# Kernel optimization log

Measured on AMD Instinct MI355X. Metric: run time of the kernel, lower is better.

The kernel has to match this reference:

```python
import jax, jax.numpy as jnp
import numpy as np

E = 16   # n_experts
K = 4    # top_k
NEG = jnp.float32(-1e20)


def _swiglu(x, w1, w2, w3):
    # bias-free SwiGLU expert: (swish(x@w1) * (x@w2)) @ w3
    a = x @ w1
    return (a * jax.nn.sigmoid(a) * (x @ w2)) @ w3


def setup_inputs() -> dict:
    key = jax.random.key(0)
    ks = jax.random.split(key, 9)
    B, S, D, H = 32, 512, 512, 1365  # H = D*2*4//3
    s = 0.02  # weight init scale to keep activations sane
    return {
        "x": jax.random.normal(ks[0], (B, S, D), jnp.float32),
        "gate_w": jax.random.normal(ks[1], (D, E), jnp.float32) * s,
        "routing_bias": jnp.zeros((E,), jnp.float32),
        "w1": jax.random.normal(ks[2], (E, D, H), jnp.float32) * s,
        "w2": jax.random.normal(ks[3], (E, D, H), jnp.float32) * s,
        "w3": jax.random.normal(ks[4], (E, H, D), jnp.float32) * s,
        "sw1": jax.random.normal(ks[5], (D, H), jnp.float32) * s,
        "sw2": jax.random.normal(ks[6], (D, H), jnp.float32) * s,
        "sw3": jax.random.normal(ks[7], (H, D), jnp.float32) * s,
    }


def reference(x, gate_w, routing_bias, w1, w2, w3, sw1, sw2, sw3):
    # gate logits + aux-free load-balancing bias  [B,S,E]
    gate_out = x @ gate_w + routing_bias
    top_v, top_i = jax.lax.top_k(gate_out, K)
    # chosen[b,s,e] = 1 if expert e is in the top-k for token (b,s)
    chosen = jax.nn.one_hot(top_i, E, dtype=x.dtype).sum(axis=-2)
    # scatter top-k values onto a -1e20 background, then softmax over experts
    masked = jnp.where(chosen > 0, gate_out, NEG)
    probs = jax.nn.softmax(masked, axis=-1)
    weights = probs * chosen  # zero outside the chosen set (matches torch mask)
    # shared expert runs on all tokens
    out = _swiglu(x, sw1, sw2, sw3)
    # per-expert SwiGLU, weighted-combined (loop over fixed small E)
    for e in range(E):
        out = out + _swiglu(x, w1[e], w2[e], w3[e]) * weights[..., e:e + 1]
    return out
```

## Files before the change

### kernel.cpp

```cpp
#include <hip/hip_runtime.h>

#define NT    16384
#define DDIM  512
#define HDIM  1365
#define HPAD  1408
#define NEXP  16
#define BK    64
#define BM    128
#define MAXTILES 656
#define MAXSLOTS 83968

typedef unsigned short u16;
typedef unsigned int   u32;
typedef __attribute__((ext_vector_type(8))) __bf16 bf16x8;
typedef __attribute__((ext_vector_type(4))) float  f32x4;
typedef __attribute__((address_space(3))) void lds_void;
typedef __attribute__((address_space(1))) void glb_void;

__device__ __forceinline__ u16 f2bf(float f) {
  union { float f; u32 u; } v; v.f = f;
  u32 u = v.u;
  u += 0x7fffu + ((u >> 16) & 1u);
  return (u16)(u >> 16);
}

__device__ __forceinline__ float bf2f(u16 b) {
  union { u32 u; float f; } v; v.u = ((u32)b) << 16;
  return v.f;
}

__device__ __forceinline__ f32x4 mfma16(bf16x8 a, bf16x8 b, f32x4 c) {
  return __builtin_amdgcn_mfma_f32_16x16x32_bf16(a, b, c, 0, 0, 0);
}

__device__ __forceinline__ void gload16(const u16* g, u16* l) {
  __builtin_amdgcn_global_load_lds((const glb_void*)g, (lds_void*)l, 16, 0, 0);
}

__device__ __forceinline__ bf16x8 lds_frag(const u16* base, int row, int e0) {
  int b = ((row << 7) + (e0 << 1)) ^ ((row & 7) << 4);
  return *(const bf16x8*)((const char*)base + b);
}

__device__ __forceinline__ int swz_n(int bid, int n) {
  int q = n >> 3, r = n & 7;
  int xcd = bid & 7, j = bid >> 3;
  return (xcd < r ? xcd * (q + 1) : r * (q + 1) + (xcd - r) * q) + j;
}

__global__ void convert_x_kernel(const float* __restrict__ in, u16* __restrict__ out, int n8) {
  int i = blockIdx.x * 256 + threadIdx.x;
  if (i >= n8) return;
  float4 a = ((const float4*)in)[2 * i];
  float4 b = ((const float4*)in)[2 * i + 1];
  u16 r[8] = {f2bf(a.x), f2bf(a.y), f2bf(a.z), f2bf(a.w),
              f2bf(b.x), f2bf(b.y), f2bf(b.z), f2bf(b.w)};
  ((uint4*)out)[i] = *(const uint4*)r;
}

__global__ void transpose12_kernel(const float* __restrict__ in, u16* __restrict__ out) {
  __shared__ float tile[32][65];
  int e = blockIdx.z;
  int h0 = blockIdx.x * 32, d0 = blockIdx.y * 64;
  int tx = threadIdx.x, ty = threadIdx.y;
  int h = h0 + tx;
#pragma unroll
  for (int r = 0; r < 8; ++r) {
    int d = d0 + ty + r * 8;
    float v = (h < HDIM) ? in[((size_t)e * DDIM + d) * HDIM + h] : 0.f;
    tile[tx][ty + r * 8] = v;
  }
  __syncthreads();
#pragma unroll
  for (int r = 0; r < 4; ++r) {
    int hh = h0 + ty + r * 8;
    u32 lo = f2bf(tile[ty + r * 8][2 * tx]);
    u32 hi = f2bf(tile[ty + r * 8][2 * tx + 1]);
    ((u32*)&out[((size_t)e * HPAD + hh) * DDIM + d0])[tx] = lo | (hi << 16);
  }
}

__global__ void transpose3_kernel(const float* __restrict__ in, u16* __restrict__ out) {
  __shared__ float tile[32][65];
  int e = blockIdx.z;
  int h0 = blockIdx.x * 64, d0 = blockIdx.y * 32;
  int tx = threadIdx.x, ty = threadIdx.y;
  int d = d0 + tx;
#pragma unroll
  for (int r = 0; r < 8; ++r) {
    int h = h0 + ty + r * 8;
    float v = (h < HDIM) ? in[((size_t)e * HDIM + h) * DDIM + d] : 0.f;
    tile[tx][ty + r * 8] = v;
  }
  __syncthreads();
#pragma unroll
  for (int r = 0; r < 4; ++r) {
    int dd = d0 + ty + r * 8;
    u32 lo = f2bf(tile[ty + r * 8][2 * tx]);
    u32 hi = f2bf(tile[ty + r * 8][2 * tx + 1]);
    ((u32*)&out[((size_t)e * DDIM + dd) * HPAD + h0])[tx] = lo | (hi << 16);
  }
}

__global__ __launch_bounds__(512) void routing_kernel(
    const float* __restrict__ x, const float* __restrict__ gw,
    const float* __restrict__ rbias,
    int* __restrict__ top_e, float* __restrict__ top_w) {
  __shared__ float gwT[NEXP * DDIM];
  int tid = threadIdx.x;
  for (int i = tid; i < NEXP * DDIM; i += 512) {
    int d = i >> 4, e = i & 15;
    gwT[e * DDIM + d] = gw[i];
  }
  __syncthreads();
  int w = tid >> 6, lane = tid & 63;
  int t = blockIdx.x * 8 + w;
  const float* xr = x + (size_t)t * DDIM;
  float xv[8];
#pragma unroll
  for (int k = 0; k < 8; ++k) xv[k] = xr[lane + (k << 6)];
  float acc[NEXP];
#pragma unroll
  for (int e = 0; e < NEXP; ++e) {
    const float* ge = gwT + e * DDIM + lane;
    float s = 0.f;
#pragma unroll
    for (int k = 0; k < 8; ++k) s += xv[k] * ge[k << 6];
#pragma unroll
    for (int off = 32; off; off >>= 1) s += __shfl_xor(s, off);
    acc[e] = s + rbias[e];
  }
  if (lane == 0) {
    int sel[4]; float sv[4];
    unsigned used = 0;
#pragma unroll
    for (int i = 0; i < 4; ++i) {
      float best = -1e30f; int bi = 0;
#pragma unroll
      for (int e = 0; e < NEXP; ++e) {
        bool ok = !((used >> e) & 1u) && acc[e] > best;
        best = ok ? acc[e] : best;
        bi   = ok ? e : bi;
      }
      used |= 1u << bi; sel[i] = bi; sv[i] = best;
    }
    float m = sv[0];
    float ex[4]; float s = 0.f;
#pragma unroll
    for (int i = 0; i < 4; ++i) { ex[i] = __expf(sv[i] - m); s += ex[i]; }
    float inv = 1.f / s;
#pragma unroll
    for (int i = 0; i < 4; ++i) {
      top_e[t * 4 + i] = sel[i];
      top_w[t * 4 + i] = ex[i] * inv;
    }
  }
}

__global__ __launch_bounds__(1024) void rank_kernel(const int* __restrict__ top_e,
                                                    int* __restrict__ counts,
                                                    int* __restrict__ top_pos) {
  __shared__ int hist[NEXP], base[NEXP];
  int tid = threadIdx.x;
  int t = blockIdx.x * 1024 + tid;
  if (tid < NEXP) hist[tid] = 0;
  __syncthreads();
  int e4[4], r4[4];
#pragma unroll
  for (int i = 0; i < 4; ++i) {
    e4[i] = top_e[t * 4 + i];
    r4[i] = atomicAdd(&hist[e4[i]], 1);
  }
  __syncthreads();
  if (tid < NEXP) base[tid] = atomicAdd(&counts[tid], hist[tid]);
  __syncthreads();
#pragma unroll
  for (int i = 0; i < 4; ++i) top_pos[t * 4 + i] = base[e4[i]] + r4[i];
}

__global__ void finalize_kernel(const int* __restrict__ counts, int* __restrict__ slot_off,
                                int* __restrict__ ntiles, int2* __restrict__ desc) {
  if (threadIdx.x != 0) return;
  int off = 0, td = 0;
  for (int e = 0; e < 17; ++e) {
    int c = (e == 16) ? NT : counts[e];
    slot_off[e] = off;
    int nt = (c + BM - 1) / BM;
    for (int i = 0; i < nt; ++i) { desc[td] = make_int2(e, off + i * BM); ++td; }
    off += nt * BM;
  }
  slot_off[17] = off;
  *ntiles = td;
}

__global__ void scatter_kernel(const int* __restrict__ top_e, const float* __restrict__ top_w,
                               const int* __restrict__ top_pos, const int* __restrict__ slot_off,
                               int* __restrict__ tok_pad, float* __restrict__ w_pad,
                               int* __restrict__ pos_list) {
  int t = blockIdx.x * 256 + threadIdx.x;
  if (t >= NT) return;
#pragma unroll
  for (int i = 0; i < 4; ++i) {
    int e = top_e[t * 4 + i];
    int slot = slot_off[e] + top_pos[t * 4 + i];
    tok_pad[slot] = t;
    w_pad[slot] = top_w[t * 4 + i];
    pos_list[t * 4 + i] = slot;
  }
  int sh = slot_off[16] + t;
  tok_pad[sh] = t;
  w_pad[sh] = 1.f;
}

__global__ __launch_bounds__(256, 3) void gemm1_kernel(
    const u16* __restrict__ x_bf, const u16* __restrict__ w1t, const u16* __restrict__ w2t,
    const u16* __restrict__ sw1t, const u16* __restrict__ sw2t,
    const int* __restrict__ ntiles, const int2* __restrict__ desc,
    const int* __restrict__ tok_pad, u16* __restrict__ h, int lo, int ntc) {
  int ti = (lo >> 7) + swz_n(blockIdx.x, ntc);
  if (ti >= *ntiles) return;
  int2 de = desc[ti];
  int e = de.x, m0 = de.y;
  int n0 = blockIdx.y * 64;
  const u16* W1 = (e == 16) ? sw1t : (w1t + (size_t)e * HPAD * DDIM);
  const u16* W2 = (e == 16) ? sw2t : (w2t + (size_t)e * HPAD * DDIM);

  __shared__ u16 smem[16384];
  u16* xs = smem;
  u16* bs = smem + 8192;

  int tid = threadIdx.x, w = tid >> 6, lane = tid & 63;
  int wm = w >> 1, wn = w & 1, lr = lane & 15, lk = lane >> 4;

  const u16* ags[4]; const u16* bgs[4];
  int ce = (((lane & 7) ^ ((lane >> 3) & 7)) << 3);
#pragma unroll
  for (int p = 0; p < 4; ++p) {
    int r = w * 32 + p * 8 + (lane >> 3);
    ags[p] = x_bf + (size_t)tok_pad[m0 + r] * DDIM + ce;
    int grp = (w * 32 + p * 8) >> 4;
    const u16* Wsrc = (grp & 1) ? W2 : W1;
    int hrow = n0 + ((grp >> 1) << 4) + (r & 15);
    bgs[p] = Wsrc + (size_t)hrow * DDIM + ce;
  }

  f32x4 acc[4][4] = {};

  for (int ks = 0; ks < DDIM / BK; ++ks) {
    int k0 = ks * BK;
#pragma unroll
    for (int p = 0; p < 4; ++p) {
      gload16(ags[p] + k0, xs + ((w * 32 + p * 8) << 6));
      gload16(bgs[p] + k0, bs + ((w * 32 + p * 8) << 6));
    }
    __syncthreads();
#pragma unroll
    for (int kf = 0; kf < 2; ++kf) {
      int e0 = kf * 32 + lk * 8;
      bf16x8 bfr[4];
#pragma unroll
      for (int nf = 0; nf < 4; ++nf)
        bfr[nf] = lds_frag(bs, wn * 64 + nf * 16 + lr, e0);
#pragma unroll
      for (int mf = 0; mf < 4; ++mf) {
        bf16x8 a = lds_frag(xs, wm * 64 + mf * 16 + lr, e0);
#pragma unroll
        for (int nf = 0; nf < 4; ++nf)
          acc[mf][nf] = mfma16(a, bfr[nf], acc[mf][nf]);
      }
    }
    __syncthreads();
  }

  u16* hs = smem;
#pragma unroll
  for (int mf = 0; mf < 4; ++mf)
#pragma unroll
    for (int nf = 0; nf < 4; nf += 2)
#pragma unroll
      for (int j = 0; j < 4; ++j) {
        float g = acc[mf][nf][j], u = acc[mf][nf + 1][j];
        float hv = g * u / (1.f + __expf(-g));
        int row = wm * 64 + mf * 16 + lk * 4 + j;
        int col = wn * 32 + (nf >> 1) * 16 + lr;
        hs[(row << 6) + col] = f2bf(hv);
      }
  __syncthreads();
#pragma unroll
  for (int i = 0; i < 4; ++i) {
    int idx = (i * 256 + tid) * 8;
    int row = idx >> 6, col = idx & 63;
    *(uint4*)&h[(size_t)(m0 - lo + row) * HPAD + n0 + col] = *(uint4*)&hs[idx];
  }
}

template <bool YMODE>
__global__ __launch_bounds__(256, 3) void gemm2_kernel(
    const u16* __restrict__ h, const u16* __restrict__ w3t, const u16* __restrict__ sw3t,
    const int* __restrict__ ntiles, const int2* __restrict__ desc,
    const int* __restrict__ tok_pad, const float* __restrict__ w_pad,
    u16* __restrict__ y, float* __restrict__ out, int lo, int ntc) {
  int ti = (lo >> 7) + swz_n(blockIdx.x, ntc);
  if (ti >= *ntiles) return;
  int2 de = desc[ti];
  int e = de.x, m0 = de.y;
  int n0 = blockIdx.y * 128;
  const u16* W3 = (e == 16) ? sw3t : (w3t + (size_t)e * DDIM * HPAD);

  __shared__ u16 smem[16384];
  __shared__ float swl[BM];
  u16* hs = smem;
  u16* ws3 = smem + 8192;

  int tid = threadIdx.x, w = tid >> 6, lane = tid & 63;
  int wm = w >> 1, wn = w & 1, lr = lane & 15, lk = lane >> 4;

  if (tid < BM) swl[tid] = w_pad[m0 + tid];

  const u16* ags[4]; const u16* bgs[4];
  int ce = (((lane & 7) ^ ((lane >> 3) & 7)) << 3);
#pragma unroll
  for (int p = 0; p < 4; ++p) {
    int r = w * 32 + p * 8 + (lane >> 3);
    ags[p] = h + (size_t)(m0 - lo + r) * HPAD + ce;
    bgs[p] = W3 + (size_t)(n0 + r) * HPAD + ce;
  }

  f32x4 acc[4][4] = {};

  for (int ks = 0; ks < HPAD / BK; ++ks) {
    int k0 = ks * BK;
#pragma unroll
    for (int p = 0; p < 4; ++p) {
      gload16(ags[p] + k0, hs + ((w * 32 + p * 8) << 6));
      gload16(bgs[p] + k0, ws3 + ((w * 32 + p * 8) << 6));
    }
    __syncthreads();
#pragma unroll
    for (int kf = 0; kf < 2; ++kf) {
      int e0 = kf * 32 + lk * 8;
      bf16x8 bfr[4];
#pragma unroll
      for (int nf = 0; nf < 4; ++nf)
        bfr[nf] = lds_frag(ws3, wn * 64 + nf * 16 + lr, e0);
#pragma unroll
      for (int mf = 0; mf < 4; ++mf) {
        bf16x8 a = lds_frag(hs, wm * 64 + mf * 16 + lr, e0);
#pragma unroll
        for (int nf = 0; nf < 4; ++nf)
          acc[mf][nf] = mfma16(a, bfr[nf], acc[mf][nf]);
      }
    }
    __syncthreads();
  }

  if constexpr (YMODE) {
    u16* ys = smem;
#pragma unroll
    for (int mf = 0; mf < 4; ++mf)
#pragma unroll
      for (int j = 0; j < 4; ++j) {
        int row = wm * 64 + mf * 16 + lk * 4 + j;
        float wv = swl[row];
#pragma unroll
        for (int nf = 0; nf < 4; ++nf)
          ys[(row << 7) + wn * 64 + nf * 16 + lr] = f2bf(acc[mf][nf][j] * wv);
      }
    __syncthreads();
#pragma unroll
    for (int i = 0; i < 8; ++i) {
      int idx = (i * 256 + tid) * 8;
      int row = idx >> 7, col = idx & 127;
      *(uint4*)&y[(size_t)(m0 + row) * DDIM + n0 + col] = *(uint4*)&ys[idx];
    }
  } else {
#pragma unroll
    for (int mf = 0; mf < 4; ++mf)
#pragma unroll
      for (int j = 0; j < 4; ++j) {
        int row = wm * 64 + mf * 16 + lk * 4 + j;
        float wv = swl[row];
        float* orow = out + (size_t)tok_pad[m0 + row] * DDIM + n0;
#pragma unroll
        for (int nf = 0; nf < 4; ++nf)
          atomicAdd(&orow[wn * 64 + nf * 16 + lr], acc[mf][nf][j] * wv);
      }
  }
}

__global__ void reduce_kernel(const u16* __restrict__ y, const int* __restrict__ pos_list,
                              const int* __restrict__ slot_off, float* __restrict__ out) {
  int t = blockIdx.x;
  int c = threadIdx.x;
  int4 pl = ((const int4*)pos_list)[t];
  int sh = slot_off[16] + t;
  ushort4 a = ((const ushort4*)(y + (size_t)sh * DDIM))[c];
  ushort4 b = ((const ushort4*)(y + (size_t)pl.x * DDIM))[c];
  ushort4 d = ((const ushort4*)(y + (size_t)pl.y * DDIM))[c];
  ushort4 e = ((const ushort4*)(y + (size_t)pl.z * DDIM))[c];
  ushort4 f = ((const ushort4*)(y + (size_t)pl.w * DDIM))[c];
  float4 s;
  s.x = bf2f(a.x) + bf2f(b.x) + bf2f(d.x) + bf2f(e.x) + bf2f(f.x);
  s.y = bf2f(a.y) + bf2f(b.y) + bf2f(d.y) + bf2f(e.y) + bf2f(f.y);
  s.z = bf2f(a.z) + bf2f(b.z) + bf2f(d.z) + bf2f(e.z) + bf2f(f.z);
  s.w = bf2f(a.w) + bf2f(b.w) + bf2f(d.w) + bf2f(e.w) + bf2f(f.w);
  ((float4*)(out + (size_t)t * DDIM))[c] = s;
}

extern "C" void kernel_launch(void* const* d_in, const int* in_sizes, int n_in,
                              void* d_out, int out_size, void* d_ws, size_t ws_size,
                              hipStream_t stream) {
  const float* x      = (const float*)d_in[0];
  const float* gate_w = (const float*)d_in[1];
  const float* rbias  = (const float*)d_in[2];
  const float* w1     = (const float*)d_in[3];
  const float* w2     = (const float*)d_in[4];
  const float* w3     = (const float*)d_in[5];
  const float* sw1    = (const float*)d_in[6];
  const float* sw2    = (const float*)d_in[7];
  const float* sw3    = (const float*)d_in[8];
  float* out = (float*)d_out;

  char* ws = (char*)d_ws;
  size_t off = 0;
  auto alloc = [&](size_t bytes) -> char* {
    char* p = ws + off;
    off += (bytes + 255) & ~(size_t)255;
    return p;
  };
  u16* x_bf  = (u16*)alloc((size_t)NT * DDIM * 2);
  u16* w1t   = (u16*)alloc((size_t)NEXP * HPAD * DDIM * 2);
  u16* w2t   = (u16*)alloc((size_t)NEXP * HPAD * DDIM * 2);
  u16* w3t   = (u16*)alloc((size_t)NEXP * DDIM * HPAD * 2);
  u16* sw1t  = (u16*)alloc((size_t)HPAD * DDIM * 2);
  u16* sw2t  = (u16*)alloc((size_t)HPAD * DDIM * 2);
  u16* sw3t  = (u16*)alloc((size_t)DDIM * HPAD * 2);
  int*   counts   = (int*)alloc(64 * 4);
  int*   top_e    = (int*)alloc((size_t)NT * 4 * 4);
  float* top_w    = (float*)alloc((size_t)NT * 4 * 4);
  int*   top_pos  = (int*)alloc((size_t)NT * 4 * 4);
  int*   slot_off = (int*)alloc(32 * 4);
  int*   ntiles   = (int*)alloc(256);
  int2*  desc     = (int2*)alloc((size_t)MAXTILES * 8);
  int*   tok_pad  = (int*)alloc((size_t)MAXSLOTS * 4);
  float* w_pad    = (float*)alloc((size_t)MAXSLOTS * 4);
  int*   pos_list = (int*)alloc((size_t)NT * 4 * 4);
  size_t y_off = off;
  u16* y = (u16*)alloc((size_t)MAXSLOTS * DDIM * 2);
  size_t h_off_y = off;
  (void)in_sizes; (void)n_in; (void)ws_size;

  const size_t per_row = (size_t)HPAD * 2;
  bool ymode;
  size_t h_off, rows_avail;
  size_t avail_y = (ws_size > h_off_y) ? (ws_size - h_off_y) : 0;
  if (avail_y / per_row >= 10496) {
    ymode = true; h_off = h_off_y; rows_avail = avail_y / per_row;
  } else {
    ymode = false; h_off = y_off;
    size_t avail_a = (ws_size > y_off) ? (ws_size - y_off) : 0;
    rows_avail = avail_a / per_row;
  }
  int CS;
  if (rows_avail >= (size_t)MAXSLOTS) CS = MAXSLOTS;
  else {
    CS = (int)((rows_avail / 2048) * 2048);
    if (CS < 2048) CS = (int)((rows_avail / BM) * BM);
    if (CS < BM) CS = BM;
  }
  int NCH = (MAXSLOTS + CS - 1) / CS;
  u16* h = (u16*)(ws + h_off);

  hipMemsetAsync(counts, 0, 64 * 4, stream);
  hipMemsetAsync(tok_pad, 0, (size_t)MAXSLOTS * 4, stream);
  hipMemsetAsync(w_pad, 0, (size_t)MAXSLOTS * 4, stream);
  if (!ymode) hipMemsetAsync(out, 0, (size_t)out_size * 4, stream);

  int n8 = NT * DDIM / 8;
  convert_x_kernel<<<n8 / 256, 256, 0, stream>>>(x, x_bf, n8);

  dim3 tb(32, 8);
  transpose12_kernel<<<dim3(HPAD / 32, DDIM / 64, NEXP), tb, 0, stream>>>(w1, w1t);
  transpose12_kernel<<<dim3(HPAD / 32, DDIM / 64, NEXP), tb, 0, stream>>>(w2, w2t);
  transpose12_kernel<<<dim3(HPAD / 32, DDIM / 64, 1),    tb, 0, stream>>>(sw1, sw1t);
  transpose12_kernel<<<dim3(HPAD / 32, DDIM / 64, 1),    tb, 0, stream>>>(sw2, sw2t);
  transpose3_kernel<<<dim3(HPAD / 64, DDIM / 32, NEXP),  tb, 0, stream>>>(w3, w3t);
  transpose3_kernel<<<dim3(HPAD / 64, DDIM / 32, 1),     tb, 0, stream>>>(sw3, sw3t);

  routing_kernel<<<NT / 8, 512, 0, stream>>>(x, gate_w, rbias, top_e, top_w);
  rank_kernel<<<NT / 1024, 1024, 0, stream>>>(top_e, counts, top_pos);
  finalize_kernel<<<1, 64, 0, stream>>>(counts, slot_off, ntiles, desc);
  scatter_kernel<<<NT / 256, 256, 0, stream>>>(top_e, top_w, top_pos, slot_off,
                                               tok_pad, w_pad, pos_list);

  for (int c = 0; c < NCH; ++c) {
    int lo = c * CS;
    int ntc = (MAXSLOTS - lo < CS ? MAXSLOTS - lo : CS) >> 7;
    gemm1_kernel<<<dim3(ntc, HPAD / 64), 256, 0, stream>>>(
        x_bf, w1t, w2t, sw1t, sw2t, ntiles, desc, tok_pad, h, lo, ntc);
    if (ymode)
      gemm2_kernel<true><<<dim3(ntc, DDIM / 128), 256, 0, stream>>>(
          h, w3t, sw3t, ntiles, desc, tok_pad, w_pad, y, out, lo, ntc);
    else
      gemm2_kernel<false><<<dim3(ntc, DDIM / 128), 256, 0, stream>>>(
          h, w3t, sw3t, ntiles, desc, tok_pad, w_pad, y, out, lo, ntc);
  }
  if (ymode) reduce_kernel<<<NT, 128, 0, stream>>>(y, pos_list, slot_off, out);
}
```

Before: 642.4 us.

## Fuse x conversion into routing, merge transpose launches, linearize GEMM grids, swizzle epilogue LDS

Folds the fp32-to-bf16 conversion of x into the routing kernel, which now reads x with vectorized loads and uses a permuted gate-weight layout in LDS. The six weight-transpose launches become two, each selecting its source tensor by blockIdx.z. The GEMM grids are flattened to 1D, and the XCD swizzle now covers every (token tile, column block) pair so neighbouring tiles sharing weights land on the same XCD. The epilogue LDS staging gets an XOR swizzle to cut bank conflicts. Together these aim to reduce launch count, global memory passes and L2 misses, at the cost of slightly more index arithmetic.

Result: faster. 615.0 us (-4.3%).

```diff
diff --git a/kernel.cpp b/kernel.cpp
--- a/kernel.cpp
+++ b/kernel.cpp
@@ -48,26 +48,24 @@
   return (xcd < r ? xcd * (q + 1) : r * (q + 1) + (xcd - r) * q) + j;
 }
 
-__global__ void convert_x_kernel(const float* __restrict__ in, u16* __restrict__ out, int n8) {
-  int i = blockIdx.x * 256 + threadIdx.x;
-  if (i >= n8) return;
-  float4 a = ((const float4*)in)[2 * i];
-  float4 b = ((const float4*)in)[2 * i + 1];
-  u16 r[8] = {f2bf(a.x), f2bf(a.y), f2bf(a.z), f2bf(a.w),
-              f2bf(b.x), f2bf(b.y), f2bf(b.z), f2bf(b.w)};
-  ((uint4*)out)[i] = *(const uint4*)r;
-}
-
-__global__ void transpose12_kernel(const float* __restrict__ in, u16* __restrict__ out) {
+__global__ void transpose12_kernel(const float* __restrict__ w1, const float* __restrict__ w2,
+                                   const float* __restrict__ sw1, const float* __restrict__ sw2,
+                                   u16* __restrict__ w1t, u16* __restrict__ w2t,
+                                   u16* __restrict__ sw1t, u16* __restrict__ sw2t) {
   __shared__ float tile[32][65];
-  int e = blockIdx.z;
+  int z = blockIdx.z;
+  const float* in; u16* out;
+  if (z < 16)      { in = w1 + (size_t)z * DDIM * HDIM;        out = w1t + (size_t)z * HPAD * DDIM; }
+  else if (z < 32) { in = w2 + (size_t)(z - 16) * DDIM * HDIM; out = w2t + (size_t)(z - 16) * HPAD * DDIM; }
+  else if (z == 32){ in = sw1; out = sw1t; }
+  else             { in = sw2; out = sw2t; }
   int h0 = blockIdx.x * 32, d0 = blockIdx.y * 64;
   int tx = threadIdx.x, ty = threadIdx.y;
   int h = h0 + tx;
 #pragma unroll
   for (int r = 0; r < 8; ++r) {
     int d = d0 + ty + r * 8;
-    float v = (h < HDIM) ? in[((size_t)e * DDIM + d) * HDIM + h] : 0.f;
+    float v = (h < HDIM) ? in[(size_t)d * HDIM + h] : 0.f;
     tile[tx][ty + r * 8] = v;
   }
   __syncthreads();
@@ -76,20 +74,23 @@
     int hh = h0 + ty + r * 8;
     u32 lo = f2bf(tile[ty + r * 8][2 * tx]);
     u32 hi = f2bf(tile[ty + r * 8][2 * tx + 1]);
-    ((u32*)&out[((size_t)e * HPAD + hh) * DDIM + d0])[tx] = lo | (hi << 16);
-  }
-}
-
-__global__ void transpose3_kernel(const float* __restrict__ in, u16* __restrict__ out) {
+    ((u32*)&out[(size_t)hh * DDIM + d0])[tx] = lo | (hi << 16);
+  }
+}
+
+__global__ void transpose3_kernel(const float* __restrict__ w3, const float* __restrict__ sw3,
+                                  u16* __restrict__ w3t, u16* __restrict__ sw3t) {
   __shared__ float tile[32][65];
-  int e = blockIdx.z;
+  int z = blockIdx.z;
+  const float* in = (z < 16) ? (w3 + (size_t)z * HDIM * DDIM) : sw3;
+  u16* out = (z < 16) ? (w3t + (size_t)z * DDIM * HPAD) : sw3t;
   int h0 = blockIdx.x * 64, d0 = blockIdx.y * 32;
   int tx = threadIdx.x, ty = threadIdx.y;
   int d = d0 + tx;
 #pragma unroll
   for (int r = 0; r < 8; ++r) {
     int h = h0 + ty + r * 8;
-    float v = (h < HDIM) ? in[((size_t)e * HDIM + h) * DDIM + d] : 0.f;
+    float v = (h < HDIM) ? in[(size_t)h * DDIM + d] : 0.f;
     tile[tx][ty + r * 8] = v;
   }
   __syncthreads();
@@ -98,31 +99,34 @@
     int dd = d0 + ty + r * 8;
     u32 lo = f2bf(tile[ty + r * 8][2 * tx]);
     u32 hi = f2bf(tile[ty + r * 8][2 * tx + 1]);
-    ((u32*)&out[((size_t)e * DDIM + dd) * HPAD + h0])[tx] = lo | (hi << 16);
+    ((u32*)&out[(size_t)dd * HPAD + h0])[tx] = lo | (hi << 16);
   }
 }
 
 __global__ __launch_bounds__(512) void routing_kernel(
     const float* __restrict__ x, const float* __restrict__ gw,
-    const float* __restrict__ rbias,
+    const float* __restrict__ rbias, u16* __restrict__ x_bf,
     int* __restrict__ top_e, float* __restrict__ top_w) {
-  __shared__ float gwT[NEXP * DDIM];
+  __shared__ float gwp[NEXP * DDIM];
   int tid = threadIdx.x;
   for (int i = tid; i < NEXP * DDIM; i += 512) {
     int d = i >> 4, e = i & 15;
-    gwT[e * DDIM + d] = gw[i];
+    gwp[e * DDIM + ((d & 7) << 6) + (d >> 3)] = gw[i];
   }
   __syncthreads();
   int w = tid >> 6, lane = tid & 63;
   int t = blockIdx.x * 8 + w;
-  const float* xr = x + (size_t)t * DDIM;
-  float xv[8];
-#pragma unroll
-  for (int k = 0; k < 8; ++k) xv[k] = xr[lane + (k << 6)];
+  const float* xr = x + (size_t)t * DDIM + lane * 8;
+  float4 xa = ((const float4*)xr)[0], xb = ((const float4*)xr)[1];
+  float xv[8] = {xa.x, xa.y, xa.z, xa.w, xb.x, xb.y, xb.z, xb.w};
+  u16 r[8];
+#pragma unroll
+  for (int k = 0; k < 8; ++k) r[k] = f2bf(xv[k]);
+  *(uint4*)&x_bf[(size_t)t * DDIM + lane * 8] = *(const uint4*)r;
   float acc[NEXP];
 #pragma unroll
   for (int e = 0; e < NEXP; ++e) {
-    const float* ge = gwT + e * DDIM + lane;
+    const float* ge = gwp + e * DDIM + lane;
     float s = 0.f;
 #pragma unroll
     for (int k = 0; k < 8; ++k) s += xv[k] * ge[k << 6];
@@ -217,11 +221,13 @@
     const u16* __restrict__ sw1t, const u16* __restrict__ sw2t,
     const int* __restrict__ ntiles, const int2* __restrict__ desc,
     const int* __restrict__ tok_pad, u16* __restrict__ h, int lo, int ntc) {
-  int ti = (lo >> 7) + swz_n(blockIdx.x, ntc);
+  int wk = swz_n(blockIdx.x, ntc * 22);
+  int tloc = wk / 22, hblk = wk - tloc * 22;
+  int ti = (lo >> 7) + tloc;
   if (ti >= *ntiles) return;
   int2 de = desc[ti];
   int e = de.x, m0 = de.y;
-  int n0 = blockIdx.y * 64;
+  int n0 = hblk * 64;
   const u16* W1 = (e == 16) ? sw1t : (w1t + (size_t)e * HPAD * DDIM);
   const u16* W2 = (e == 16) ? sw2t : (w2t + (size_t)e * HPAD * DDIM);
 
@@ -283,14 +289,15 @@
         float hv = g * u / (1.f + __expf(-g));
         int row = wm * 64 + mf * 16 + lk * 4 + j;
         int col = wn * 32 + (nf >> 1) * 16 + lr;
-        hs[(row << 6) + col] = f2bf(hv);
+        hs[((row << 6) + col) ^ ((row & 7) << 3)] = f2bf(hv);
       }
   __syncthreads();
 #pragma unroll
   for (int i = 0; i < 4; ++i) {
     int idx = (i * 256 + tid) * 8;
     int row = idx >> 6, col = idx & 63;
-    *(uint4*)&h[(size_t)(m0 - lo + row) * HPAD + n0 + col] = *(uint4*)&hs[idx];
+    *(uint4*)&h[(size_t)(m0 - lo + row) * HPAD + n0 + col] =
+        *(uint4*)&hs[idx ^ ((row & 7) << 3)];
   }
 }
 
@@ -300,11 +307,13 @@
     const int* __restrict__ ntiles, const int2* __restrict__ desc,
     const int* __restrict__ tok_pad, const float* __restrict__ w_pad,
     u16* __restrict__ y, float* __restrict__ out, int lo, int ntc) {
-  int ti = (lo >> 7) + swz_n(blockIdx.x, ntc);
+  int wk = swz_n(blockIdx.x, ntc * 4);
+  int tloc = wk >> 2, dblk = wk & 3;
+  int ti = (lo >> 7) + tloc;
   if (ti >= *ntiles) return;
   int2 de = desc[ti];
   int e = de.x, m0 = de.y;
-  int n0 = blockIdx.y * 128;
+  int n0 = dblk * 128;
   const u16* W3 = (e == 16) ? sw3t : (w3t + (size_t)e * DDIM * HPAD);
 
   __shared__ u16 smem[16384];
@@ -364,14 +373,16 @@
         float wv = swl[row];
 #pragma unroll
         for (int nf = 0; nf < 4; ++nf)
-          ys[(row << 7) + wn * 64 + nf * 16 + lr] = f2bf(acc[mf][nf][j] * wv);
+          ys[((row << 7) + wn * 64 + nf * 16 + lr) ^ ((row & 7) << 3)] =
+              f2bf(acc[mf][nf][j] * wv);
       }
     __syncthreads();
 #pragma unroll
     for (int i = 0; i < 8; ++i) {
       int idx = (i * 256 + tid) * 8;
       int row = idx >> 7, col = idx & 127;
-      *(uint4*)&y[(size_t)(m0 + row) * DDIM + n0 + col] = *(uint4*)&ys[idx];
+      *(uint4*)&y[(size_t)(m0 + row) * DDIM + n0 + col] =
+          *(uint4*)&smem[idx ^ ((row & 7) << 3)];
     }
   } else {
 #pragma unroll
@@ -476,18 +487,13 @@
   hipMemsetAsync(w_pad, 0, (size_t)MAXSLOTS * 4, stream);
   if (!ymode) hipMemsetAsync(out, 0, (size_t)out_size * 4, stream);
 
-  int n8 = NT * DDIM / 8;
-  convert_x_kernel<<<n8 / 256, 256, 0, stream>>>(x, x_bf, n8);
-
   dim3 tb(32, 8);
-  transpose12_kernel<<<dim3(HPAD / 32, DDIM / 64, NEXP), tb, 0, stream>>>(w1, w1t);
-  transpose12_kernel<<<dim3(HPAD / 32, DDIM / 64, NEXP), tb, 0, stream>>>(w2, w2t);
-  transpose12_kernel<<<dim3(HPAD / 32, DDIM / 64, 1),    tb, 0, stream>>>(sw1, sw1t);
-  transpose12_kernel<<<dim3(HPAD / 32, DDIM / 64, 1),    tb, 0, stream>>>(sw2, sw2t);
-  transpose3_kernel<<<dim3(HPAD / 64, DDIM / 32, NEXP),  tb, 0, stream>>>(w3, w3t);
-  transpose3_kernel<<<dim3(HPAD / 64, DDIM / 32, 1),     tb, 0, stream>>>(sw3, sw3t);
-
-  routing_kernel<<<NT / 8, 512, 0, stream>>>(x, gate_w, rbias, top_e, top_w);
+  transpose12_kernel<<<dim3(HPAD / 32, DDIM / 64, 34), tb, 0, stream>>>(
+      w1, w2, sw1, sw2, w1t, w2t, sw1t, sw2t);
+  transpose3_kernel<<<dim3(HPAD / 64, DDIM / 32, 17), tb, 0, stream>>>(
+      w3, sw3, w3t, sw3t);
+
+  routing_kernel<<<NT / 8, 512, 0, stream>>>(x, gate_w, rbias, x_bf, top_e, top_w);
   rank_kernel<<<NT / 1024, 1024, 0, stream>>>(top_e, counts, top_pos);
   finalize_kernel<<<1, 64, 0, stream>>>(counts, slot_off, ntiles, desc);
   scatter_kernel<<<NT / 256, 256, 0, stream>>>(top_e, top_w, top_pos, slot_off,
@@ -496,13 +502,13 @@
   for (int c = 0; c < NCH; ++c) {
     int lo = c * CS;
     int ntc = (MAXSLOTS - lo < CS ? MAXSLOTS - lo : CS) >> 7;
-    gemm1_kernel<<<dim3(ntc, HPAD / 64), 256, 0, stream>>>(
+    gemm1_kernel<<<ntc * 22, 256, 0, stream>>>(
         x_bf, w1t, w2t, sw1t, sw2t, ntiles, desc, tok_pad, h, lo, ntc);
     if (ymode)
-      gemm2_kernel<true><<<dim3(ntc, DDIM / 128), 256, 0, stream>>>(
+      gemm2_kernel<true><<<ntc * 4, 256, 0, stream>>>(
           h, w3t, sw3t, ntiles, desc, tok_pad, w_pad, y, out, lo, ntc);
     else
-      gemm2_kernel<false><<<dim3(ntc, DDIM / 128), 256, 0, stream>>>(
+      gemm2_kernel<false><<<ntc * 4, 256, 0, stream>>>(
           h, w3t, sw3t, ntiles, desc, tok_pad, w_pad, y, out, lo, ntc);
   }
   if (ymode) reduce_kernel<<<NT, 128, 0, stream>>>(y, pos_list, slot_off, out);
```
